# Kernel tuning notes

Hardware: AMD Instinct MI355X
Metric: run time of the kernel (lower is better)

Reference implementation:

```python
import jax, jax.numpy as jnp
import numpy as np

B, P, D, N = 32, 3, 300, 2048

def setup_inputs() -> dict:
    key = jax.random.key(0)
    k1, k2 = jax.random.split(key)
    input_data1 = jax.random.normal(k1, (B, P, D, N), dtype=jnp.float32)
    input_data2 = jax.random.normal(k2, (B, P, D, N), dtype=jnp.float32)
    return {"input_data1": input_data1, "input_data2": input_data2}

def reference(input_data1, input_data2):
    # Horizontal comparison: permute(0,1,3,2) -> vectors of length D at each
    # (batch, pool, position); compute cos, l2, l1 distance per vector pair.
    x = jnp.transpose(input_data1, (0, 1, 3, 2))  # [B,P,N,D]
    y = jnp.transpose(input_data2, (0, 1, 3, 2))  # [B,P,N,D]
    dot = jnp.sum(x * y, axis=-1)
    xn = jnp.sqrt(jnp.sum(x * x, axis=-1))
    yn = jnp.sqrt(jnp.sum(y * y, axis=-1))
    cos = dot / (xn * yn)                      # [B,P,N]
    d = x - y
    l2 = jnp.sqrt(jnp.sum(d * d, axis=-1))     # [B,P,N]
    l1 = jnp.sum(jnp.abs(d), axis=-1)          # [B,P,N]  (sqrt((x-y)^2).sum())
    out = jnp.stack([cos, l2, l1], axis=-1)    # [B,P,N,3]
    b = out.shape[0]
    return out.reshape(b, -1, out.shape[-1])   # [B, P*N, 3]
```

## Files before the change

### kernel.cpp

```cpp
#include <hip/hip_runtime.h>
#include <math.h>


constexpr int kB = 32;
constexpr int kP = 3;
constexpr int kD = 300;
constexpr int kN = 2048;

__global__ __launch_bounds__(256) void sim_measure_kernel(
    const float* __restrict__ x,
    const float* __restrict__ y,
    float* __restrict__ out)
{
    const int tid = blockIdx.x * 256 + threadIdx.x;
    const int total = kB * kP * kN;
    if (tid >= total) return;

    const int n  = tid & (kN - 1);
    const int bp = tid >> 11;

    const size_t base = (size_t)bp * kD * kN + n;
    const float* __restrict__ xp = x + base;
    const float* __restrict__ yp = y + base;

    float dot = 0.f, xx = 0.f, yy = 0.f, l2s = 0.f, l1 = 0.f;

    #pragma unroll 4
    for (int d = 0; d < kD; ++d) {
        const float xv = xp[(size_t)d * kN];
        const float yv = yp[(size_t)d * kN];
        dot = fmaf(xv, yv, dot);
        xx  = fmaf(xv, xv, xx);
        yy  = fmaf(yv, yv, yy);
        const float df = xv - yv;
        l2s = fmaf(df, df, l2s);
        l1 += fabsf(df);
    }

    const float cosv = dot / (sqrtf(xx) * sqrtf(yy));
    const float l2v  = sqrtf(l2s);

    const size_t o = (size_t)tid * 3;
    out[o + 0] = cosv;
    out[o + 1] = l2v;
    out[o + 2] = l1;
}

extern "C" void kernel_launch(void* const* d_in, const int* in_sizes, int n_in,
                              void* d_out, int out_size, void* d_ws, size_t ws_size,
                              hipStream_t stream)
{
    const float* x = (const float*)d_in[0];
    const float* y = (const float*)d_in[1];
    float* out = (float*)d_out;

    const int total = kB * kP * kN;
    const int block = 256;
    const int grid  = (total + block - 1) / block;

    sim_measure_kernel<<<grid, block, 0, stream>>>(x, y, out);
}
```

Baseline: 467.4 us.

## Split D across lane groups with float4 loads and shuffle reduction

Each wave now covers 64 consecutive positions. Each lane handles 4 adjacent positions through float4 loads. The four 16-lane groups each accumulate a quarter of the D dimension, and the partial sums are merged with wave shuffles. Results are packed into three float4 stores per lane group. The goal is more memory-level parallelism and wider transactions for a bandwidth-bound reduction, at the cost of extra shuffle work and more accumulator registers.

```diff
diff --git a/kernel.cpp b/kernel.cpp
--- a/kernel.cpp
+++ b/kernel.cpp
@@ -6,44 +6,79 @@
 constexpr int kP = 3;
 constexpr int kD = 300;
 constexpr int kN = 2048;
+constexpr int kSeg = 4;
+constexpr int kDSeg = kD / kSeg;
+
+__device__ inline void reduce4(float4& v) {
+    v.x += __shfl_down(v.x, 32); v.y += __shfl_down(v.y, 32);
+    v.z += __shfl_down(v.z, 32); v.w += __shfl_down(v.w, 32);
+    v.x += __shfl_down(v.x, 16); v.y += __shfl_down(v.y, 16);
+    v.z += __shfl_down(v.z, 16); v.w += __shfl_down(v.w, 16);
+}
 
 __global__ __launch_bounds__(256) void sim_measure_kernel(
     const float* __restrict__ x,
     const float* __restrict__ y,
     float* __restrict__ out)
 {
-    const int tid = blockIdx.x * 256 + threadIdx.x;
-    const int total = kB * kP * kN;
-    if (tid >= total) return;
+    const int tid  = blockIdx.x * 256 + threadIdx.x;
+    const int lane = tid & 63;
+    const int wave = tid >> 6;
 
-    const int n  = tid & (kN - 1);
-    const int bp = tid >> 11;
+    const int q = lane & 15;
+    const int s = lane >> 4;
 
-    const size_t base = (size_t)bp * kD * kN + n;
-    const float* __restrict__ xp = x + base;
-    const float* __restrict__ yp = y + base;
+    const int bp = wave >> 5;
+    const int n0 = (wave & 31) << 6;
 
-    float dot = 0.f, xx = 0.f, yy = 0.f, l2s = 0.f, l1 = 0.f;
+    const size_t base = ((size_t)bp * kD + (size_t)s * kDSeg) * kN + (size_t)(n0 + q * 4);
+    const float4* __restrict__ xp = (const float4*)(x + base);
+    const float4* __restrict__ yp = (const float4*)(y + base);
+    constexpr int kStride4 = kN / 4;
 
-    #pragma unroll 4
-    for (int d = 0; d < kD; ++d) {
-        const float xv = xp[(size_t)d * kN];
-        const float yv = yp[(size_t)d * kN];
-        dot = fmaf(xv, yv, dot);
-        xx  = fmaf(xv, xv, xx);
-        yy  = fmaf(yv, yv, yy);
-        const float df = xv - yv;
-        l2s = fmaf(df, df, l2s);
-        l1 += fabsf(df);
+    float4 dot = {0.f, 0.f, 0.f, 0.f};
+    float4 xx  = {0.f, 0.f, 0.f, 0.f};
+    float4 yy  = {0.f, 0.f, 0.f, 0.f};
+    float4 l2s = {0.f, 0.f, 0.f, 0.f};
+    float4 l1  = {0.f, 0.f, 0.f, 0.f};
+
+    #pragma unroll 5
+    for (int d = 0; d < kDSeg; ++d) {
+        const float4 xv = xp[(size_t)d * kStride4];
+        const float4 yv = yp[(size_t)d * kStride4];
+
+        dot.x = fmaf(xv.x, yv.x, dot.x); dot.y = fmaf(xv.y, yv.y, dot.y);
+        dot.z = fmaf(xv.z, yv.z, dot.z); dot.w = fmaf(xv.w, yv.w, dot.w);
+        xx.x  = fmaf(xv.x, xv.x, xx.x);  xx.y  = fmaf(xv.y, xv.y, xx.y);
+        xx.z  = fmaf(xv.z, xv.z, xx.z);  xx.w  = fmaf(xv.w, xv.w, xx.w);
+        yy.x  = fmaf(yv.x, yv.x, yy.x);  yy.y  = fmaf(yv.y, yv.y, yy.y);
+        yy.z  = fmaf(yv.z, yv.z, yy.z);  yy.w  = fmaf(yv.w, yv.w, yy.w);
+        const float dx = xv.x - yv.x, dy = xv.y - yv.y,
+                    dz = xv.z - yv.z, dw = xv.w - yv.w;
+        l2s.x = fmaf(dx, dx, l2s.x); l2s.y = fmaf(dy, dy, l2s.y);
+        l2s.z = fmaf(dz, dz, l2s.z); l2s.w = fmaf(dw, dw, l2s.w);
+        l1.x += fabsf(dx); l1.y += fabsf(dy);
+        l1.z += fabsf(dz); l1.w += fabsf(dw);
     }
 
-    const float cosv = dot / (sqrtf(xx) * sqrtf(yy));
-    const float l2v  = sqrtf(l2s);
+    reduce4(dot); reduce4(xx); reduce4(yy); reduce4(l2s); reduce4(l1);
 
-    const size_t o = (size_t)tid * 3;
-    out[o + 0] = cosv;
-    out[o + 1] = l2v;
-    out[o + 2] = l1;
+    if (s == 0) {
+        float4 o0, o1, o2;
+        const float c0 = dot.x / (sqrtf(xx.x) * sqrtf(yy.x));
+        const float c1 = dot.y / (sqrtf(xx.y) * sqrtf(yy.y));
+        const float c2 = dot.z / (sqrtf(xx.z) * sqrtf(yy.z));
+        const float c3 = dot.w / (sqrtf(xx.w) * sqrtf(yy.w));
+        const float e0 = sqrtf(l2s.x), e1 = sqrtf(l2s.y),
+                    e2 = sqrtf(l2s.z), e3 = sqrtf(l2s.w);
+
+        o0.x = c0;   o0.y = e0;   o0.z = l1.x; o0.w = c1;
+        o1.x = e1;   o1.y = l1.y; o1.z = c2;   o1.w = e2;
+        o2.x = l1.z; o2.y = c3;   o2.z = e3;   o2.w = l1.w;
+
+        float4* op = (float4*)(out + ((size_t)bp * kN + (size_t)(n0 + q * 4)) * 3);
+        op[0] = o0; op[1] = o1; op[2] = o2;
+    }
 }
 
 extern "C" void kernel_launch(void* const* d_in, const int* in_sizes, int n_in,
@@ -56,7 +91,7 @@
 
     const int total = kB * kP * kN;
     const int block = 256;
-    const int grid  = (total + block - 1) / block;
+    const int grid  = total / block;
 
     sim_measure_kernel<<<grid, block, 0, stream>>>(x, y, out);
 }
```

Result: faster. 451.3 us (-3.4%).

## Split D reduction across threads with float4 loads and shared-memory reduce

Applied to the files above, without the earlier changes.

Each block now covers 64 positions, with 16 thread groups each striding over a slice of the D dimension and loading float4 vectors. Partial sums are combined with wave shuffles and shared memory, and the results are written with vectorized float4 stores. The aim is more memory-level parallelism and better occupancy than the old one-thread-per-position serial loop over 300 strided loads. The cost is extra reduction and synchronisation overhead.

```diff
diff --git a/kernel.cpp b/kernel.cpp
--- a/kernel.cpp
+++ b/kernel.cpp
@@ -6,44 +6,95 @@
 constexpr int kP = 3;
 constexpr int kD = 300;
 constexpr int kN = 2048;
+constexpr int kStride4 = kN / 4;
 
-__global__ __launch_bounds__(256) void sim_measure_kernel(
+__device__ inline void fma4(float4& a, const float4 u, const float4 v) {
+    a.x = fmaf(u.x, v.x, a.x); a.y = fmaf(u.y, v.y, a.y);
+    a.z = fmaf(u.z, v.z, a.z); a.w = fmaf(u.w, v.w, a.w);
+}
+__device__ inline void red2(float4& v) {
+    v.x += __shfl_down(v.x, 32); v.y += __shfl_down(v.y, 32);
+    v.z += __shfl_down(v.z, 32); v.w += __shfl_down(v.w, 32);
+    v.x += __shfl_down(v.x, 16); v.y += __shfl_down(v.y, 16);
+    v.z += __shfl_down(v.z, 16); v.w += __shfl_down(v.w, 16);
+}
+
+__global__ __launch_bounds__(256, 8) void sim_measure_kernel(
     const float* __restrict__ x,
     const float* __restrict__ y,
     float* __restrict__ out)
 {
-    const int tid = blockIdx.x * 256 + threadIdx.x;
-    const int total = kB * kP * kN;
-    if (tid >= total) return;
+    __shared__ float4 sm[4 * 16 * 5];
 
-    const int n  = tid & (kN - 1);
-    const int bp = tid >> 11;
+    const int tid = threadIdx.x;
+    const int q   = tid & 15;
+    const int s   = tid >> 4;
+    const int bp  = blockIdx.x >> 5;
+    const int n0  = (blockIdx.x & 31) << 6;
 
-    const size_t base = (size_t)bp * kD * kN + n;
-    const float* __restrict__ xp = x + base;
-    const float* __restrict__ yp = y + base;
+    const size_t base = (size_t)bp * kD * kN + (size_t)(n0 + q * 4);
+    const float4* __restrict__ xp = (const float4*)(x + base);
+    const float4* __restrict__ yp = (const float4*)(y + base);
 
-    float dot = 0.f, xx = 0.f, yy = 0.f, l2s = 0.f, l1 = 0.f;
+    float4 dot = {0,0,0,0}, xx = {0,0,0,0}, yy = {0,0,0,0},
+           l2s = {0,0,0,0}, l1 = {0,0,0,0};
 
-    #pragma unroll 4
-    for (int d = 0; d < kD; ++d) {
-        const float xv = xp[(size_t)d * kN];
-        const float yv = yp[(size_t)d * kN];
-        dot = fmaf(xv, yv, dot);
-        xx  = fmaf(xv, xv, xx);
-        yy  = fmaf(yv, yv, yy);
-        const float df = xv - yv;
-        l2s = fmaf(df, df, l2s);
-        l1 += fabsf(df);
+    float4 xv = xp[(size_t)s * kStride4];
+    float4 yv = yp[(size_t)s * kStride4];
+    for (int d = s + 16; d < kD; d += 16) {
+        const float4 xn = xp[(size_t)d * kStride4];
+        const float4 yn = yp[(size_t)d * kStride4];
+        fma4(dot, xv, yv); fma4(xx, xv, xv); fma4(yy, yv, yv);
+        float4 df = {xv.x - yv.x, xv.y - yv.y, xv.z - yv.z, xv.w - yv.w};
+        fma4(l2s, df, df);
+        l1.x += fabsf(df.x); l1.y += fabsf(df.y);
+        l1.z += fabsf(df.z); l1.w += fabsf(df.w);
+        xv = xn; yv = yn;
+    }
+    fma4(dot, xv, yv); fma4(xx, xv, xv); fma4(yy, yv, yv);
+    {
+        float4 df = {xv.x - yv.x, xv.y - yv.y, xv.z - yv.z, xv.w - yv.w};
+        fma4(l2s, df, df);
+        l1.x += fabsf(df.x); l1.y += fabsf(df.y);
+        l1.z += fabsf(df.z); l1.w += fabsf(df.w);
     }
 
-    const float cosv = dot / (sqrtf(xx) * sqrtf(yy));
-    const float l2v  = sqrtf(l2s);
+    red2(dot); red2(xx); red2(yy); red2(l2s); red2(l1);
 
-    const size_t o = (size_t)tid * 3;
-    out[o + 0] = cosv;
-    out[o + 1] = l2v;
-    out[o + 2] = l1;
+    const int wv = tid >> 6;
+    if ((tid & 63) < 16) {
+        const int qq = tid & 15;
+        float4* p = &sm[(wv * 16 + qq) * 5];
+        p[0] = dot; p[1] = xx; p[2] = yy; p[3] = l2s; p[4] = l1;
+    }
+    __syncthreads();
+
+    if (tid < 16) {
+        float4 D = {0,0,0,0}, X = {0,0,0,0}, Y = {0,0,0,0},
+               E = {0,0,0,0}, A = {0,0,0,0};
+        #pragma unroll
+        for (int w = 0; w < 4; ++w) {
+            const float4* p = &sm[(w * 16 + tid) * 5];
+            float4 a = p[0], b = p[1], c = p[2], e = p[3], f = p[4];
+            D.x += a.x; D.y += a.y; D.z += a.z; D.w += a.w;
+            X.x += b.x; X.y += b.y; X.z += b.z; X.w += b.w;
+            Y.x += c.x; Y.y += c.y; Y.z += c.z; Y.w += c.w;
+            E.x += e.x; E.y += e.y; E.z += e.z; E.w += e.w;
+            A.x += f.x; A.y += f.y; A.z += f.z; A.w += f.w;
+        }
+        const float c0 = D.x / (sqrtf(X.x) * sqrtf(Y.x));
+        const float c1 = D.y / (sqrtf(X.y) * sqrtf(Y.y));
+        const float c2 = D.z / (sqrtf(X.z) * sqrtf(Y.z));
+        const float c3 = D.w / (sqrtf(X.w) * sqrtf(Y.w));
+        const float e0 = sqrtf(E.x), e1 = sqrtf(E.y),
+                    e2 = sqrtf(E.z), e3 = sqrtf(E.w);
+
+        float4 o0 = {c0,  e0,  A.x, c1};
+        float4 o1 = {e1,  A.y, c2,  e2};
+        float4 o2 = {A.z, c3,  e3,  A.w};
+        float4* op = (float4*)(out + ((size_t)bp * kN + (size_t)(n0 + tid * 4)) * 3);
+        op[0] = o0; op[1] = o1; op[2] = o2;
+    }
 }
 
 extern "C" void kernel_launch(void* const* d_in, const int* in_sizes, int n_in,
@@ -54,9 +105,6 @@
     const float* y = (const float*)d_in[1];
     float* out = (float*)d_out;
 
-    const int total = kB * kP * kN;
-    const int block = 256;
-    const int grid  = (total + block - 1) / block;
-
-    sim_measure_kernel<<<grid, block, 0, stream>>>(x, y, out);
+    const int grid = kB * kP * (kN / 64);
+    sim_measure_kernel<<<grid, 256, 0, stream>>>(x, y, out);
 }
```

Measured after the change: 459.4 us. About the same (-1.7%).
